# Kernel tuning notes

Measured on AMD Instinct MI355X. Metric: run time of the kernel, lower is better.

The kernel has to match this reference:

```python
import jax, jax.numpy as jnp
import numpy as np

WIN = 9  # local window size per spatial dim

def _boxfilter3d(x):
    k = jnp.ones((1, 1, WIN, WIN, WIN), x.dtype) / float(WIN ** 3)
    return jax.lax.conv_general_dilated(
        x, k, window_strides=(1, 1, 1), padding='SAME',
        dimension_numbers=('NCDHW', 'OIDHW', 'NCDHW'))

def setup_inputs() -> dict:
    key = jax.random.key(0)
    k1, k2 = jax.random.split(key)
    shape = (2, 1, 160, 192, 160)
    y_true = jax.random.uniform(k1, shape, dtype=jnp.float32)
    y_pred = jax.random.uniform(k2, shape, dtype=jnp.float32)
    return {"y_true": y_true, "y_pred": y_pred}

def reference(y_true, y_pred):
    Ii, Ji = y_true, y_pred
    mu1 = _boxfilter3d(Ii)
    mu2 = _boxfilter3d(Ji)
    sigma1_sq = _boxfilter3d(Ii * Ii) - mu1 * mu1
    sigma2_sq = _boxfilter3d(Ji * Ji) - mu2 * mu2
    sigma12 = _boxfilter3d(Ii * Ji) - mu1 * mu2
    cc = (sigma12 * sigma12) / (sigma1_sq * sigma2_sq + 1e-5)
    return -jnp.mean(cc)
```

## Files before the change

### kernel.cpp

```cpp
#include <hip/hip_runtime.h>

#define DD 160
#define HH 192
#define WW 160
#define HWs (HH * WW)
#define NTOT 9830400.0f
#define DOUT 40
#define NIT  48
#define NBLK 480

typedef float    v4 __attribute__((ext_vector_type(4)));
typedef float    v8 __attribute__((ext_vector_type(8)));
typedef _Float16 h4 __attribute__((ext_vector_type(4)));
typedef _Float16 h8 __attribute__((ext_vector_type(8)));

__global__ __launch_bounds__(256, 2) void kf(const float* __restrict__ I,
                                             const float* __restrict__ J,
                                             float* __restrict__ partial) {
    __shared__ float rawb[2][2][24][40];
    __shared__ h4    hsb[2][5][16][10];
    __shared__ h8    ring[9][5][64];

    const int tid = threadIdx.x;
    const int bx  = blockIdx.x;
    const int b   = blockIdx.z;
    const int tx  = bx % 5, ty = bx / 5;
    const int w0 = tx * 32, h0 = ty * 16;
    const int d0 = blockIdx.y * DOUT;
    const int bid = bx + 60 * (blockIdx.y + 4 * b);

    const int  rtid = tid ^ ((bx & 1) << 7);
    const bool isW  = (rtid >= 192);
    const bool isH  = (rtid < 160);
    const int  p    = rtid & 63;
    const int  wr   = p >> 2, wg8 = p & 3;
    const int  hr   = rtid / 10, hk = rtid % 10;

    const int  uA   = tid;
    const int  qA   = (uA < 240) ? uA : uA - 240;
    const int  inpA = (uA < 240) ? 0 : 1;
    const int  rowA = qA / 10, gA = qA % 10;
    const int  ghA = h0 - 4 + rowA, gwA = w0 - 4 + gA * 4;
    const bool okA = (ghA >= 0 && ghA < HH && gwA >= 0 && gwA < WW);
    const size_t offA = (size_t)ghA * WW + gwA;
    const int  ldsA = inpA * 960 + rowA * 40 + gA * 4;
    const float* srcA = inpA ? J : I;

    const bool hasB = (tid < 224);
    const int  qB   = tid + 16;
    const int  rowB = qB / 10, gB = qB % 10;
    const int  ghB = h0 - 4 + rowB, gwB = w0 - 4 + gB * 4;
    const bool okB = hasB && (ghB >= 0 && ghB < HH && gwB >= 0 && gwB < WW);
    const size_t offB = (size_t)ghB * WW + gwB;
    const int  ldsB = 960 + rowB * 40 + gB * 4;

    float* rawF = &rawb[0][0][0][0];
    const size_t base_b = (size_t)b * DD * HWs;

    v4 pA = (v4)0.f, pB = (v4)0.f;
    {
        const int s0 = d0 - 4;
        if (s0 >= 0) {
            const size_t sb = base_b + (size_t)s0 * HWs;
            if (okA) pA = *(const v4*)(srcA + sb + offA);
            if (okB) pB = *(const v4*)(J + sb + offB);
        }
    }

    v8 S[5] = {(v8)0.f, (v8)0.f, (v8)0.f, (v8)0.f, (v8)0.f};
    v8 accv = (v8)0.f;
    int wslot = 0;
    const float inv = 1.0f / 729.0f;

    for (int t = 0; t <= NIT; ++t) {
        const int  si  = d0 - 4 + t;
        const bool sv  = (t < NIT) && (si >= 0 && si < DD);
        const int  par = t & 1;

        if (sv) {
            *(v4*)(rawF + par * 1920 + ldsA) = pA;
            if (hasB) *(v4*)(rawF + par * 1920 + ldsB) = pB;
        }
        if (t + 1 < NIT) {
            const int sn = si + 1;
            if (sn >= 0 && sn < DD) {
                const size_t sb = base_b + (size_t)sn * HWs;
                pA = okA ? *(const v4*)(srcA + sb + offA) : (v4)0.f;
                if (hasB) pB = okB ? *(const v4*)(J + sb + offB) : (v4)0.f;
            }
        }
        __syncthreads();

        if (sv && isH) {
            v4 sI = (v4)0.f, sJ = (v4)0.f, sII = (v4)0.f, sJJ = (v4)0.f,
               sIJ = (v4)0.f;
#pragma unroll
            for (int tt = 0; tt < 9; ++tt) {
                v4 a  = *(const v4*)&rawb[par][0][hr + tt][hk * 4];
                v4 bb = *(const v4*)&rawb[par][1][hr + tt][hk * 4];
                sI += a; sJ += bb; sII += a * a; sJJ += bb * bb; sIJ += a * bb;
            }
            hsb[par][0][hr][hk] = __builtin_convertvector(sI,  h4);
            hsb[par][1][hr][hk] = __builtin_convertvector(sJ,  h4);
            hsb[par][2][hr][hk] = __builtin_convertvector(sII, h4);
            hsb[par][3][hr][hk] = __builtin_convertvector(sJJ, h4);
            hsb[par][4][hr][hk] = __builtin_convertvector(sIJ, h4);
        }

        if (t >= 1 && isW) {
            const int tp  = t - 1;
            const int sip = d0 - 4 + tp;
            v8 o[5];
            if (sip >= 0 && sip < DD) {
                const int pb = tp & 1;
#pragma unroll
                for (int c = 0; c < 5; ++c) {
                    const h4* hp = &hsb[pb][c][wr][wg8 * 2];
                    v8 fa = __builtin_convertvector(*(const h8*)hp, v8);
                    v8 fb = __builtin_convertvector(*(const h8*)(hp + 2), v8);
                    float s = fa[0] + fa[1] + fa[2] + fa[3] + fa[4] + fa[5] +
                              fa[6] + fa[7] + fb[0];
                    v8 ov; ov[0] = s;
                    s = s - fa[0] + fb[1]; ov[1] = s;
                    s = s - fa[1] + fb[2]; ov[2] = s;
                    s = s - fa[2] + fb[3]; ov[3] = s;
                    s = s - fa[3] + fb[4]; ov[4] = s;
                    s = s - fa[4] + fb[5]; ov[5] = s;
                    s = s - fa[5] + fb[6]; ov[6] = s;
                    s = s - fa[6] + fb[7]; ov[7] = s;
                    o[c] = ov;
                }
            } else {
#pragma unroll
                for (int c = 0; c < 5; ++c) o[c] = (v8)0.f;
            }
#pragma unroll
            for (int c = 0; c < 5; ++c) {
                h8 nv = __builtin_convertvector(o[c], h8);
                if (tp >= 9)
                    S[c] -= __builtin_convertvector(ring[wslot][c][p], v8);
                ring[wslot][c][p] = nv;
                S[c] += __builtin_convertvector(nv, v8);
            }
            if (++wslot == 9) wslot = 0;

            if (tp >= 8) {
                v8 mu1 = S[0] * inv, mu2 = S[1] * inv;
                v8 g1  = S[2] * inv - mu1 * mu1;
                v8 g2  = S[3] * inv - mu2 * mu2;
                v8 g12 = S[4] * inv - mu1 * mu2;
                v8 num = g12 * g12;
                v8 den = g1 * g2 + 1e-5f;
#pragma unroll
                for (int e = 0; e < 8; ++e)
                    accv[e] += __fdividef(num[e], den[e]);
            }
        }
    }

    if (isW) {
        float a = accv[0] + accv[1] + accv[2] + accv[3] +
                  accv[4] + accv[5] + accv[6] + accv[7];
#pragma unroll
        for (int off = 32; off > 0; off >>= 1) a += __shfl_down(a, off);
        if (p == 0) partial[bid] = a;
    }
}

__global__ void k3_final(const float* __restrict__ partial,
                         float* __restrict__ out) {
    __shared__ float r[512];
    const int i = threadIdx.x;
    r[i] = (i < NBLK) ? partial[i] : 0.f;
    __syncthreads();
    for (int off = 256; off > 0; off >>= 1) {
        if (i < off) r[i] += r[i + off];
        __syncthreads();
    }
    if (i == 0) out[0] = -r[0] * (1.0f / NTOT);
}

extern "C" void kernel_launch(void* const* d_in, const int* in_sizes, int n_in,
                              void* d_out, int out_size, void* d_ws, size_t ws_size,
                              hipStream_t stream) {
    (void)in_sizes; (void)n_in; (void)out_size; (void)ws_size;
    const float* I = (const float*)d_in[0];
    const float* J = (const float*)d_in[1];
    float* out     = (float*)d_out;
    float* partial = (float*)d_ws;

    dim3 grid(60, 4, 2);
    kf<<<grid, 256, 0, stream>>>(I, J, partial);
    k3_final<<<1, 512, 0, stream>>>(partial, out);
}
```

Measured before the change: 163.5 us.

## Restructure box filter as depth-first running sums with smaller depth tiles

```diff
diff --git a/kernel.cpp b/kernel.cpp
--- a/kernel.cpp
+++ b/kernel.cpp
@@ -5,175 +5,160 @@
 #define WW 160
 #define HWs (HH * WW)
 #define NTOT 9830400.0f
-#define DOUT 40
-#define NIT  48
-#define NBLK 480
+#define DOUT 20
+#define NIT  28
+#define NBLK 960
+
+#define SDS 11
+#define SDC (24 * SDS)
+#define HSS 11
+#define HSC (16 * HSS)
 
 typedef float    v4 __attribute__((ext_vector_type(4)));
-typedef float    v8 __attribute__((ext_vector_type(8)));
 typedef _Float16 h4 __attribute__((ext_vector_type(4)));
-typedef _Float16 h8 __attribute__((ext_vector_type(8)));
 
-__global__ __launch_bounds__(256, 2) void kf(const float* __restrict__ I,
+__device__ __forceinline__ void block_sync_lds() {
+    __builtin_amdgcn_s_waitcnt(0xc07f);
+    __builtin_amdgcn_s_barrier();
+}
+__device__ __forceinline__ v4 up(h4 x) { return __builtin_convertvector(x, v4); }
+__device__ __forceinline__ h4 dn(v4 x) { return __builtin_convertvector(x, h4); }
+
+__global__ __launch_bounds__(256, 4) void kf(const float* __restrict__ I,
                                              const float* __restrict__ J,
                                              float* __restrict__ partial) {
-    __shared__ float rawb[2][2][24][40];
-    __shared__ h4    hsb[2][5][16][10];
-    __shared__ h8    ring[9][5][64];
+    __shared__ h4    SDL[5 * SDC];
+    __shared__ h4    HSL[5 * HSC];
+    __shared__ float red[128];
 
     const int tid = threadIdx.x;
-    const int bx  = blockIdx.x;
-    const int b   = blockIdx.z;
-    const int tx  = bx % 5, ty = bx / 5;
-    const int w0 = tx * 32, h0 = ty * 16;
-    const int d0 = blockIdx.y * DOUT;
-    const int bid = bx + 60 * (blockIdx.y + 4 * b);
+    const int bx = blockIdx.x, by = blockIdx.y, b = blockIdx.z;
+    const int w0 = (bx % 5) * 32, h0 = (bx / 5) * 16;
+    const int d0 = by * DOUT;
+    const int bid = bx + 60 * (by + 8 * b);
 
-    const int  rtid = tid ^ ((bx & 1) << 7);
-    const bool isW  = (rtid >= 192);
-    const bool isH  = (rtid < 160);
-    const int  p    = rtid & 63;
-    const int  wr   = p >> 2, wg8 = p & 3;
-    const int  hr   = rtid / 10, hk = rtid % 10;
+    const bool p1 = tid < 240;
+    const int r = tid / 10, g = tid % 10;
+    const int gh = h0 - 4 + r, gw = w0 - 4 + g * 4;
+    const bool colOK = p1 && gh >= 0 && gh < HH && gw >= 0 && gw < WW;
+    const size_t colOff = (size_t)gh * WW + gw;
+    const float* Ib = I + (size_t)b * DD * HWs + colOff;
+    const float* Jb = J + (size_t)b * DD * HWs + colOff;
+    h4* const sdw = &SDL[r * SDS + g];
 
-    const int  uA   = tid;
-    const int  qA   = (uA < 240) ? uA : uA - 240;
-    const int  inpA = (uA < 240) ? 0 : 1;
-    const int  rowA = qA / 10, gA = qA % 10;
-    const int  ghA = h0 - 4 + rowA, gwA = w0 - 4 + gA * 4;
-    const bool okA = (ghA >= 0 && ghA < HH && gwA >= 0 && gwA < WW);
-    const size_t offA = (size_t)ghA * WW + gwA;
-    const int  ldsA = inpA * 960 + rowA * 40 + gA * 4;
-    const float* srcA = inpA ? J : I;
+    const bool p2 = tid < 100;
+    const int g2 = tid % 10, q2 = tid / 10;
+    const int ch2 = q2 >> 1, hh0 = (q2 & 1) * 8;
+    const h4* const sdr = &SDL[ch2 * SDC + hh0 * SDS + g2];
+    h4* const hsw = &HSL[ch2 * HSC + hh0 * HSS + g2];
 
-    const bool hasB = (tid < 224);
-    const int  qB   = tid + 16;
-    const int  rowB = qB / 10, gB = qB % 10;
-    const int  ghB = h0 - 4 + rowB, gwB = w0 - 4 + gB * 4;
-    const bool okB = hasB && (ghB >= 0 && ghB < HH && gwB >= 0 && gwB < WW);
-    const size_t offB = (size_t)ghB * WW + gwB;
-    const int  ldsB = 960 + rowB * 40 + gB * 4;
+    const bool p3 = tid < 128;
+    const int hh = tid >> 3, sg = tid & 7;
+    const h4* const hsr = &HSL[hh * HSS + sg];
 
-    float* rawF = &rawb[0][0][0][0];
-    const size_t base_b = (size_t)b * DD * HWs;
+    v4 sd0 = 0.f, sd1 = 0.f, sd2 = 0.f, sd3 = 0.f, sd4 = 0.f;
+    h4 fI[9], fJ[9];
+#pragma unroll
+    for (int u = 0; u < 9; ++u) { fI[u] = (h4)(_Float16)0; fJ[u] = (h4)(_Float16)0; }
+    v4 pLI = 0.f, pLJ = 0.f;
+    float acc = 0.f;
+    const float inv = 1.0f / 729.0f;
 
-    v4 pA = (v4)0.f, pB = (v4)0.f;
     {
-        const int s0 = d0 - 4;
-        if (s0 >= 0) {
-            const size_t sb = base_b + (size_t)s0 * HWs;
-            if (okA) pA = *(const v4*)(srcA + sb + offA);
-            if (okB) pB = *(const v4*)(J + sb + offB);
+        const int si = d0 - 4;
+        if (colOK && si >= 0) {
+            pLI = *(const v4*)(Ib + (size_t)si * HWs);
+            pLJ = *(const v4*)(Jb + (size_t)si * HWs);
         }
     }
 
-    v8 S[5] = {(v8)0.f, (v8)0.f, (v8)0.f, (v8)0.f, (v8)0.f};
-    v8 accv = (v8)0.f;
-    int wslot = 0;
-    const float inv = 1.0f / 729.0f;
-
-    for (int t = 0; t <= NIT; ++t) {
-        const int  si  = d0 - 4 + t;
-        const bool sv  = (t < NIT) && (si >= 0 && si < DD);
-        const int  par = t & 1;
-
-        if (sv) {
-            *(v4*)(rawF + par * 1920 + ldsA) = pA;
-            if (hasB) *(v4*)(rawF + par * 1920 + ldsB) = pB;
-        }
-        if (t + 1 < NIT) {
-            const int sn = si + 1;
-            if (sn >= 0 && sn < DD) {
-                const size_t sb = base_b + (size_t)sn * HWs;
-                pA = okA ? *(const v4*)(srcA + sb + offA) : (v4)0.f;
-                if (hasB) pB = okB ? *(const v4*)(J + sb + offB) : (v4)0.f;
-            }
-        }
-        __syncthreads();
-
-        if (sv && isH) {
-            v4 sI = (v4)0.f, sJ = (v4)0.f, sII = (v4)0.f, sJJ = (v4)0.f,
-               sIJ = (v4)0.f;
+    for (int tb = 0; tb < NIT; tb += 9) {
 #pragma unroll
-            for (int tt = 0; tt < 9; ++tt) {
-                v4 a  = *(const v4*)&rawb[par][0][hr + tt][hk * 4];
-                v4 bb = *(const v4*)&rawb[par][1][hr + tt][hk * 4];
-                sI += a; sJ += bb; sII += a * a; sJJ += bb * bb; sIJ += a * bb;
-            }
-            hsb[par][0][hr][hk] = __builtin_convertvector(sI,  h4);
-            hsb[par][1][hr][hk] = __builtin_convertvector(sJ,  h4);
-            hsb[par][2][hr][hk] = __builtin_convertvector(sII, h4);
-            hsb[par][3][hr][hk] = __builtin_convertvector(sJJ, h4);
-            hsb[par][4][hr][hk] = __builtin_convertvector(sIJ, h4);
-        }
-
-        if (t >= 1 && isW) {
-            const int tp  = t - 1;
-            const int sip = d0 - 4 + tp;
-            v8 o[5];
-            if (sip >= 0 && sip < DD) {
-                const int pb = tp & 1;
+        for (int u = 0; u < 9; ++u) {
+            const int t = tb + u;
+            if (t < NIT) {
+                const int si = d0 - 4 + t;
+                if (p1) {
+                    h4 cI = dn(pLI), cJ = dn(pLJ);
+                    v4 aI = up(cI), aJ = up(cJ);
+                    v4 dI = aI, dJv = aJ;
+                    v4 dII = aI * aI, dJJ = aJ * aJ, dIJ = aI * aJ;
+                    if (t >= 9) {
+                        v4 bI = up(fI[u]), bJ = up(fJ[u]);
+                        dI -= bI; dJv -= bJ;
+                        dII -= bI * bI; dJJ -= bJ * bJ; dIJ -= bI * bJ;
+                    }
+                    fI[u] = cI; fJ[u] = cJ;
+                    sd0 += dI; sd1 += dJv; sd2 += dII; sd3 += dJJ; sd4 += dIJ;
+                    sdw[0]       = dn(sd0);
+                    sdw[SDC]     = dn(sd1);
+                    sdw[2 * SDC] = dn(sd2);
+                    sdw[3 * SDC] = dn(sd3);
+                    sdw[4 * SDC] = dn(sd4);
+                    pLI = 0.f; pLJ = 0.f;
+                    const int sn = si + 1;
+                    if (t + 1 < NIT && colOK && sn >= 0 && sn < DD) {
+                        pLI = *(const v4*)(Ib + (size_t)sn * HWs);
+                        pLJ = *(const v4*)(Jb + (size_t)sn * HWs);
+                    }
+                }
+                block_sync_lds();
+                if (p2) {
+                    v4 s = 0.f;
 #pragma unroll
-                for (int c = 0; c < 5; ++c) {
-                    const h4* hp = &hsb[pb][c][wr][wg8 * 2];
-                    v8 fa = __builtin_convertvector(*(const h8*)hp, v8);
-                    v8 fb = __builtin_convertvector(*(const h8*)(hp + 2), v8);
-                    float s = fa[0] + fa[1] + fa[2] + fa[3] + fa[4] + fa[5] +
-                              fa[6] + fa[7] + fb[0];
-                    v8 ov; ov[0] = s;
-                    s = s - fa[0] + fb[1]; ov[1] = s;
-                    s = s - fa[1] + fb[2]; ov[2] = s;
-                    s = s - fa[2] + fb[3]; ov[3] = s;
-                    s = s - fa[3] + fb[4]; ov[4] = s;
-                    s = s - fa[4] + fb[5]; ov[5] = s;
-                    s = s - fa[5] + fb[6]; ov[6] = s;
-                    s = s - fa[6] + fb[7]; ov[7] = s;
-                    o[c] = ov;
+                    for (int k = 0; k < 9; ++k) s += up(sdr[k * SDS]);
+                    hsw[0] = dn(s);
+#pragma unroll
+                    for (int j2 = 1; j2 < 8; ++j2) {
+                        s += up(sdr[(j2 + 8) * SDS]) - up(sdr[(j2 - 1) * SDS]);
+                        hsw[j2 * HSS] = dn(s);
+                    }
                 }
-            } else {
+                block_sync_lds();
+                if (p3 && t >= 8) {
+                    float w[5][4];
 #pragma unroll
-                for (int c = 0; c < 5; ++c) o[c] = (v8)0.f;
-            }
+                    for (int c = 0; c < 5; ++c) {
+                        v4 fa = up(hsr[c * HSC]);
+                        v4 fb = up(hsr[c * HSC + 1]);
+                        v4 fc = up(hsr[c * HSC + 2]);
+                        float s = fa[0] + fa[1] + fa[2] + fa[3] +
+                                  fb[0] + fb[1] + fb[2] + fb[3] + fc[0];
+                        w[c][0] = s;
+                        s += fc[1] - fa[0]; w[c][1] = s;
+                        s += fc[2] - fa[1]; w[c][2] = s;
+                        s += fc[3] - fa[2]; w[c][3] = s;
+                    }
 #pragma unroll
-            for (int c = 0; c < 5; ++c) {
-                h8 nv = __builtin_convertvector(o[c], h8);
-                if (tp >= 9)
-                    S[c] -= __builtin_convertvector(ring[wslot][c][p], v8);
-                ring[wslot][c][p] = nv;
-                S[c] += __builtin_convertvector(nv, v8);
-            }
-            if (++wslot == 9) wslot = 0;
-
-            if (tp >= 8) {
-                v8 mu1 = S[0] * inv, mu2 = S[1] * inv;
-                v8 g1  = S[2] * inv - mu1 * mu1;
-                v8 g2  = S[3] * inv - mu2 * mu2;
-                v8 g12 = S[4] * inv - mu1 * mu2;
-                v8 num = g12 * g12;
-                v8 den = g1 * g2 + 1e-5f;
-#pragma unroll
-                for (int e = 0; e < 8; ++e)
-                    accv[e] += __fdividef(num[e], den[e]);
+                    for (int e = 0; e < 4; ++e) {
+                        float mu1 = w[0][e] * inv, mu2 = w[1][e] * inv;
+                        float g1  = fmaf(-mu1, mu1, w[2][e] * inv);
+                        float g2v = fmaf(-mu2, mu2, w[3][e] * inv);
+                        float g12 = fmaf(-mu1, mu2, w[4][e] * inv);
+                        acc += __fdividef(g12 * g12, fmaf(g1, g2v, 1e-5f));
+                    }
+                }
             }
         }
     }
 
-    if (isW) {
-        float a = accv[0] + accv[1] + accv[2] + accv[3] +
-                  accv[4] + accv[5] + accv[6] + accv[7];
+    if (p3) red[tid] = acc;
+    __syncthreads();
+    if (tid < 64) {
+        float a = red[tid] + red[tid + 64];
 #pragma unroll
         for (int off = 32; off > 0; off >>= 1) a += __shfl_down(a, off);
-        if (p == 0) partial[bid] = a;
+        if (tid == 0) partial[bid] = a;
     }
 }
 
 __global__ void k3_final(const float* __restrict__ partial,
                          float* __restrict__ out) {
-    __shared__ float r[512];
+    __shared__ float r[1024];
     const int i = threadIdx.x;
     r[i] = (i < NBLK) ? partial[i] : 0.f;
     __syncthreads();
-    for (int off = 256; off > 0; off >>= 1) {
+    for (int off = 512; off > 0; off >>= 1) {
         if (i < off) r[i] += r[i + off];
         __syncthreads();
     }
@@ -189,7 +174,7 @@
     float* out     = (float*)d_out;
     float* partial = (float*)d_ws;
 
-    dim3 grid(60, 4, 2);
+    dim3 grid(60, 8, 2);
     kf<<<grid, 256, 0, stream>>>(I, J, partial);
-    k3_final<<<1, 512, 0, stream>>>(partial, out);
+    k3_final<<<1, 1024, 0, stream>>>(partial, out);
 }
```

Result: faster. 153.3 us (-6.3%).
